# Kernel optimization log

Hardware: AMD Instinct MI355X
Metric: run time of the kernel (lower is better)

The kernel has to match this reference:

```python
import jax, jax.numpy as jnp
import numpy as np

N, F_IN, UNITS, HEADS = 4096, 128, 64, 4
EDGE_P = 0.01  # adjacency density


def setup_inputs() -> dict:
    key = jax.random.key(0)
    k1, k2, k3, k4, k5 = jax.random.split(key, 5)
    inputs = jax.random.normal(k1, (N, F_IN), dtype=jnp.float32)
    adj = jax.random.bernoulli(k2, EDGE_P, (N, N)).astype(jnp.float32)
    # glorot-normal-ish parameter scales
    w = jax.random.normal(k3, (F_IN, UNITS), dtype=jnp.float32) * np.float32(np.sqrt(2.0 / (F_IN + UNITS)))
    attn_w1 = jax.random.normal(k4, (UNITS, HEADS), dtype=jnp.float32) * np.float32(np.sqrt(2.0 / (UNITS + HEADS)))
    attn_w2 = jax.random.normal(k5, (UNITS, HEADS), dtype=jnp.float32) * np.float32(np.sqrt(2.0 / (UNITS + HEADS)))
    return {"inputs": inputs, "adj": adj, "w": w, "attn_w1": attn_w1, "attn_w2": attn_w2}


def reference(inputs, adj, w, attn_w1, attn_w2):
    # dropout=0, bias=0, final_layer=False, activation=relu
    x = inputs @ w                                  # [N, U]
    e1 = x @ attn_w1                                # [N, H]
    e2 = x @ attn_w2                                # [N, H]
    # coeffs[i, j, h] = relu(e1[i, h] + e2[j, h])
    coeffs = jax.nn.relu(e1[:, None, :] + e2[None, :, :])   # [N, N, H]
    # NOTE: original multiplies by adj (zeros -> logit 0, not -inf) then softmax over j
    scores = adj[:, :, None] * coeffs               # [N, N, H]
    attn = jax.nn.softmax(scores, axis=1)           # normalize over neighbors j
    # per-head aggregation, concat heads -> [N, H*U] (head-major blocks)
    out = jnp.einsum("ijh,ju->ihu", attn, x).reshape(N, HEADS * UNITS)
    return jax.nn.relu(out)
```

## Files before the change

kernel.cpp:

```cpp
#include <hip/hip_runtime.h>

#define N_NODES 4096
#define F_IN    128
#define UNITS   64
#define HEADS   4
#define ROWS_PB 4
#define GRID1   (N_NODES / ROWS_PB)
#define NBR_CAP 128

__global__ __launch_bounds__(256, 4) void k1(
        const float* __restrict__ inputs, const float* __restrict__ adj,
        const float* __restrict__ w, const float* __restrict__ aw1,
        const float* __restrict__ aw2, float* __restrict__ x,
        float* __restrict__ e1g, float* __restrict__ e2g,
        float* __restrict__ S, int* __restrict__ cnt_g,
        unsigned short* __restrict__ nbr_g)
{
    __shared__ float w_lds[F_IN * UNITS];
    __shared__ float in_lds[ROWS_PB * F_IN];
    __shared__ float x_lds[ROWS_PB * 65];
    __shared__ unsigned short nbr_lds[ROWS_PB * NBR_CAP];

    const int t    = threadIdx.x;
    const int lane = t & 63;
    const int wid  = t >> 6;
    const int row0 = blockIdx.x * ROWS_PB;
    const int r    = row0 + wid;

    {
        const float4* src = (const float4*)w;
        float4* dst = (float4*)w_lds;
        for (int idx = t; idx < F_IN * UNITS / 4; idx += 256) dst[idx] = src[idx];
    }
    if (t < ROWS_PB * F_IN / 4)
        ((float4*)in_lds)[t] = ((const float4*)(inputs + (size_t)row0 * F_IN))[t];
    __syncthreads();

    const float4* arow = (const float4*)(adj + (size_t)r * N_NODES);
    float4 av[16];
#pragma unroll
    for (int j = 0; j < 16; j++) av[j] = arow[lane + 64 * j];

    float acc = 0.f;
    const float4* ir = (const float4*)(in_lds + wid * F_IN);
#pragma unroll 8
    for (int c = 0; c < F_IN / 4; c++) {
        const float4 a = ir[c];
        const int k4 = c * 4;
        acc = fmaf(a.x, w_lds[(k4 + 0) * UNITS + lane],
              fmaf(a.y, w_lds[(k4 + 1) * UNITS + lane],
              fmaf(a.z, w_lds[(k4 + 2) * UNITS + lane],
              fmaf(a.w, w_lds[(k4 + 3) * UNITS + lane], acc))));
    }
    x_lds[wid * 65 + lane] = acc;
    x[(size_t)r * UNITS + lane] = acc;

    int off = 0;
    const unsigned long long lt = (1ull << lane) - 1ull;
#pragma unroll
    for (int j = 0; j < 16; j++) {
        const int gbase = 4 * (lane + 64 * j);
        unsigned long long bm;
        bm = __ballot(av[j].x != 0.f);
        if (av[j].x != 0.f) { const int p = off + __popcll(bm & lt);
            if (p < NBR_CAP) nbr_lds[wid * NBR_CAP + p] = (unsigned short)(gbase + 0); }
        off += __popcll(bm);
        bm = __ballot(av[j].y != 0.f);
        if (av[j].y != 0.f) { const int p = off + __popcll(bm & lt);
            if (p < NBR_CAP) nbr_lds[wid * NBR_CAP + p] = (unsigned short)(gbase + 1); }
        off += __popcll(bm);
        bm = __ballot(av[j].z != 0.f);
        if (av[j].z != 0.f) { const int p = off + __popcll(bm & lt);
            if (p < NBR_CAP) nbr_lds[wid * NBR_CAP + p] = (unsigned short)(gbase + 2); }
        off += __popcll(bm);
        bm = __ballot(av[j].w != 0.f);
        if (av[j].w != 0.f) { const int p = off + __popcll(bm & lt);
            if (p < NBR_CAP) nbr_lds[wid * NBR_CAP + p] = (unsigned short)(gbase + 3); }
        off += __popcll(bm);
    }
    const int cntc = min(off, NBR_CAP);
    if (lane == 0) cnt_g[r] = cntc;
    for (int idx = lane; idx < cntc; idx += 64)
        nbr_g[(size_t)r * NBR_CAP + idx] = nbr_lds[wid * NBR_CAP + idx];

    __syncthreads();

    if (t < 32) {
        const int rr = t >> 3;
        const int rem = t & 7;
        const int h = rem & 3;
        const bool first = rem < 4;
        const float* aw = first ? aw1 : aw2;
        float s = 0.f;
#pragma unroll 8
        for (int uu = 0; uu < UNITS; uu++)
            s += x_lds[rr * 65 + uu] * aw[uu * HEADS + h];
        (first ? e1g : e2g)[(size_t)(row0 + rr) * HEADS + h] = s;
    }
    if (t < 64) {
        const float s = x_lds[0 * 65 + t] + x_lds[1 * 65 + t]
                      + x_lds[2 * 65 + t] + x_lds[3 * 65 + t];
        atomicAdd(&S[t], s);
    }
}

__global__ __launch_bounds__(256) void k2(
        const float* __restrict__ x, const float* __restrict__ e1g,
        const float* __restrict__ e2g, const float* __restrict__ S,
        const int* __restrict__ cnt_g, const unsigned short* __restrict__ nbr_g,
        float* __restrict__ out)
{
    __shared__ unsigned short nb[NBR_CAP];
    __shared__ float4 wgt[NBR_CAP];
    __shared__ float red[4][HEADS * UNITS];
    __shared__ float4 denred[4];

    const int i = blockIdx.x;
    const int t = threadIdx.x;
    const int lane = t & 63;
    const int wid = t >> 6;

    const int n = min(cnt_g[i], NBR_CAP);
    const float4 e1v = *(const float4*)(e1g + (size_t)i * HEADS);

    if (t < n) {
        const int j = nbr_g[(size_t)i * NBR_CAP + t];
        nb[t] = (unsigned short)j;
        const float4 e2v = *(const float4*)(e2g + (size_t)j * HEADS);
        float4 wv;
        wv.x = __expf(fmaxf(e1v.x + e2v.x, 0.f)) - 1.f;
        wv.y = __expf(fmaxf(e1v.y + e2v.y, 0.f)) - 1.f;
        wv.z = __expf(fmaxf(e1v.z + e2v.z, 0.f)) - 1.f;
        wv.w = __expf(fmaxf(e1v.w + e2v.w, 0.f)) - 1.f;
        wgt[t] = wv;
    }
    __syncthreads();

    float a0 = 0.f, a1 = 0.f, a2 = 0.f, a3 = 0.f;
    float dx = 0.f, dy = 0.f, dz = 0.f, dw = 0.f;
    for (int k = wid; k < n; k += 4) {
        const float4 p = wgt[k];
        const int j = nb[k];
        const float xv = x[(j << 6) + lane];
        a0 = fmaf(p.x, xv, a0);
        a1 = fmaf(p.y, xv, a1);
        a2 = fmaf(p.z, xv, a2);
        a3 = fmaf(p.w, xv, a3);
        dx += p.x; dy += p.y; dz += p.z; dw += p.w;
    }
    red[wid][0 * 64 + lane] = a0;
    red[wid][1 * 64 + lane] = a1;
    red[wid][2 * 64 + lane] = a2;
    red[wid][3 * 64 + lane] = a3;
    if (lane == 0) denred[wid] = make_float4(dx, dy, dz, dw);
    __syncthreads();

    const float accsum = red[0][t] + red[1][t] + red[2][t] + red[3][t];
    const float den = ((const float*)&denred[0])[wid]
                    + ((const float*)&denred[1])[wid]
                    + ((const float*)&denred[2])[wid]
                    + ((const float*)&denred[3])[wid];
    out[(size_t)i * (HEADS * UNITS) + t] =
        fmaxf((S[lane] + accsum) / ((float)N_NODES + den), 0.f);
}

extern "C" void kernel_launch(void* const* d_in, const int* in_sizes, int n_in,
                              void* d_out, int out_size, void* d_ws, size_t ws_size,
                              hipStream_t stream) {
    const float* inputs = (const float*)d_in[0];
    const float* adj    = (const float*)d_in[1];
    const float* w      = (const float*)d_in[2];
    const float* aw1    = (const float*)d_in[3];
    const float* aw2    = (const float*)d_in[4];
    float* out = (float*)d_out;

    float* ws = (float*)d_ws;
    float* x   = ws;
    float* e1  = ws + 262144;
    float* e2  = ws + 262144 + 16384;
    float* S   = ws + 262144 + 2 * 16384;
    int*   cnt = (int*)(ws + 262144 + 2 * 16384 + 64);
    unsigned short* nbr = (unsigned short*)(ws + 262144 + 2 * 16384 + 64 + 4096);

    hipMemsetAsync(S, 0, UNITS * sizeof(float), stream);
    k1<<<GRID1, 256, 0, stream>>>(inputs, adj, w, aw1, aw2, x, e1, e2, S, cnt, nbr);
    k2<<<N_NODES, 256, 0, stream>>>(x, e1, e2, S, cnt, nbr, out);
}
```

Baseline: 137.5 us.

## Split projection and adjacency scan into interleaved heterogeneous blocks

The first kernel now runs two kinds of blocks in one grid. One in five blocks does the 4-row feature projection plus the attention-logit and column-sum work. The other blocks each compact the neighbour list of a single adjacency row using all 256 threads, with a shared atomic counter assigning offsets per wave. The aim is to spread the large adjacency read over more, shorter blocks and decouple it from the GEMM work. The cost is that each block still reserves the shared-memory union sized for the GEMM path, so fewer adjacency rows may be in flight per CU. Neighbour order inside a row also becomes nondeterministic across waves.

```diff
diff --git a/kernel.cpp b/kernel.cpp
--- a/kernel.cpp
+++ b/kernel.cpp
@@ -5,10 +5,14 @@
 #define UNITS   64
 #define HEADS   4
 #define ROWS_PB 4
-#define GRID1   (N_NODES / ROWS_PB)
+#define GRID_GEMM (N_NODES / ROWS_PB)
+#define GRID_A  (GRID_GEMM + N_NODES)
 #define NBR_CAP 128
 
-__global__ __launch_bounds__(256, 4) void k1(
+struct GemmS { float w[F_IN * UNITS]; float in[ROWS_PB * F_IN]; float xl[ROWS_PB * 65]; };
+struct ScanS { unsigned short nbr[NBR_CAP]; };
+
+__global__ __launch_bounds__(256) void kA(
         const float* __restrict__ inputs, const float* __restrict__ adj,
         const float* __restrict__ w, const float* __restrict__ aw1,
         const float* __restrict__ aw2, float* __restrict__ x,
@@ -16,95 +20,121 @@
         float* __restrict__ S, int* __restrict__ cnt_g,
         unsigned short* __restrict__ nbr_g)
 {
-    __shared__ float w_lds[F_IN * UNITS];
-    __shared__ float in_lds[ROWS_PB * F_IN];
-    __shared__ float x_lds[ROWS_PB * 65];
-    __shared__ unsigned short nbr_lds[ROWS_PB * NBR_CAP];
-
+    __shared__ union { GemmS g; ScanS s; } u;
+    __shared__ int cnt;
+
+    const int bid  = blockIdx.x;
     const int t    = threadIdx.x;
     const int lane = t & 63;
     const int wid  = t >> 6;
-    const int row0 = blockIdx.x * ROWS_PB;
-    const int r    = row0 + wid;
-
-    {
-        const float4* src = (const float4*)w;
-        float4* dst = (float4*)w_lds;
-        for (int idx = t; idx < F_IN * UNITS / 4; idx += 256) dst[idx] = src[idx];
-    }
-    if (t < ROWS_PB * F_IN / 4)
-        ((float4*)in_lds)[t] = ((const float4*)(inputs + (size_t)row0 * F_IN))[t];
-    __syncthreads();
-
-    const float4* arow = (const float4*)(adj + (size_t)r * N_NODES);
-    float4 av[16];
-#pragma unroll
-    for (int j = 0; j < 16; j++) av[j] = arow[lane + 64 * j];
-
-    float acc = 0.f;
-    const float4* ir = (const float4*)(in_lds + wid * F_IN);
+
+    if (bid % 5 == 0) {
+        const int row0 = (bid / 5) * ROWS_PB;
+
+        {
+            const float4* src = (const float4*)w;
+            float4* dst = (float4*)u.g.w;
+            for (int idx = t; idx < F_IN * UNITS / 4; idx += 256) dst[idx] = src[idx];
+        }
+        if (t < ROWS_PB * F_IN / 4)
+            ((float4*)u.g.in)[t] = ((const float4*)(inputs + (size_t)row0 * F_IN))[t];
+        __syncthreads();
+
+        float acc = 0.f;
+        const float4* ir = (const float4*)(u.g.in + wid * F_IN);
 #pragma unroll 8
-    for (int c = 0; c < F_IN / 4; c++) {
-        const float4 a = ir[c];
-        const int k4 = c * 4;
-        acc = fmaf(a.x, w_lds[(k4 + 0) * UNITS + lane],
-              fmaf(a.y, w_lds[(k4 + 1) * UNITS + lane],
-              fmaf(a.z, w_lds[(k4 + 2) * UNITS + lane],
-              fmaf(a.w, w_lds[(k4 + 3) * UNITS + lane], acc))));
-    }
-    x_lds[wid * 65 + lane] = acc;
-    x[(size_t)r * UNITS + lane] = acc;
-
-    int off = 0;
-    const unsigned long long lt = (1ull << lane) - 1ull;
-#pragma unroll
-    for (int j = 0; j < 16; j++) {
-        const int gbase = 4 * (lane + 64 * j);
-        unsigned long long bm;
-        bm = __ballot(av[j].x != 0.f);
-        if (av[j].x != 0.f) { const int p = off + __popcll(bm & lt);
-            if (p < NBR_CAP) nbr_lds[wid * NBR_CAP + p] = (unsigned short)(gbase + 0); }
-        off += __popcll(bm);
-        bm = __ballot(av[j].y != 0.f);
-        if (av[j].y != 0.f) { const int p = off + __popcll(bm & lt);
-            if (p < NBR_CAP) nbr_lds[wid * NBR_CAP + p] = (unsigned short)(gbase + 1); }
-        off += __popcll(bm);
-        bm = __ballot(av[j].z != 0.f);
-        if (av[j].z != 0.f) { const int p = off + __popcll(bm & lt);
-            if (p < NBR_CAP) nbr_lds[wid * NBR_CAP + p] = (unsigned short)(gbase + 2); }
-        off += __popcll(bm);
-        bm = __ballot(av[j].w != 0.f);
-        if (av[j].w != 0.f) { const int p = off + __popcll(bm & lt);
-            if (p < NBR_CAP) nbr_lds[wid * NBR_CAP + p] = (unsigned short)(gbase + 3); }
-        off += __popcll(bm);
-    }
-    const int cntc = min(off, NBR_CAP);
-    if (lane == 0) cnt_g[r] = cntc;
-    for (int idx = lane; idx < cntc; idx += 64)
-        nbr_g[(size_t)r * NBR_CAP + idx] = nbr_lds[wid * NBR_CAP + idx];
-
-    __syncthreads();
-
-    if (t < 32) {
-        const int rr = t >> 3;
-        const int rem = t & 7;
-        const int h = rem & 3;
-        const bool first = rem < 4;
-        const float* aw = first ? aw1 : aw2;
-        float s = 0.f;
+        for (int c = 0; c < F_IN / 4; c++) {
+            const float4 a = ir[c];
+            const int k4 = c * 4;
+            acc = fmaf(a.x, u.g.w[(k4 + 0) * UNITS + lane],
+                  fmaf(a.y, u.g.w[(k4 + 1) * UNITS + lane],
+                  fmaf(a.z, u.g.w[(k4 + 2) * UNITS + lane],
+                  fmaf(a.w, u.g.w[(k4 + 3) * UNITS + lane], acc))));
+        }
+        u.g.xl[wid * 65 + lane] = acc;
+        x[(size_t)(row0 + wid) * UNITS + lane] = acc;
+        __syncthreads();
+
+        if (t < 32) {
+            const int rr = t >> 3;
+            const int rem = t & 7;
+            const int h = rem & 3;
+            const bool first = rem < 4;
+            const float* aw = first ? aw1 : aw2;
+            float s = 0.f;
 #pragma unroll 8
-        for (int uu = 0; uu < UNITS; uu++)
-            s += x_lds[rr * 65 + uu] * aw[uu * HEADS + h];
-        (first ? e1g : e2g)[(size_t)(row0 + rr) * HEADS + h] = s;
-    }
-    if (t < 64) {
-        const float s = x_lds[0 * 65 + t] + x_lds[1 * 65 + t]
-                      + x_lds[2 * 65 + t] + x_lds[3 * 65 + t];
-        atomicAdd(&S[t], s);
+            for (int uu = 0; uu < UNITS; uu++)
+                s += u.g.xl[rr * 65 + uu] * aw[uu * HEADS + h];
+            (first ? e1g : e2g)[(size_t)(row0 + rr) * HEADS + h] = s;
+        }
+        if (t < 64) {
+            const float s = u.g.xl[0 * 65 + t] + u.g.xl[1 * 65 + t]
+                          + u.g.xl[2 * 65 + t] + u.g.xl[3 * 65 + t];
+            atomicAdd(&S[t], s);
+        }
+    } else {
+        const int i = bid - bid / 5 - 1;
+
+        if (t == 0) cnt = 0;
+        __syncthreads();
+
+        const float4* arow = (const float4*)(adj + (size_t)i * N_NODES);
+        const float4 v0 = arow[t];
+        const float4 v1 = arow[t + 256];
+        const float4 v2 = arow[t + 512];
+        const float4 v3 = arow[t + 768];
+
+        const unsigned long long b0  = __ballot(v0.x != 0.f);
+        const unsigned long long b1  = __ballot(v0.y != 0.f);
+        const unsigned long long b2  = __ballot(v0.z != 0.f);
+        const unsigned long long b3  = __ballot(v0.w != 0.f);
+        const unsigned long long b4  = __ballot(v1.x != 0.f);
+        const unsigned long long b5  = __ballot(v1.y != 0.f);
+        const unsigned long long b6  = __ballot(v1.z != 0.f);
+        const unsigned long long b7  = __ballot(v1.w != 0.f);
+        const unsigned long long b8  = __ballot(v2.x != 0.f);
+        const unsigned long long b9  = __ballot(v2.y != 0.f);
+        const unsigned long long b10 = __ballot(v2.z != 0.f);
+        const unsigned long long b11 = __ballot(v2.w != 0.f);
+        const unsigned long long b12 = __ballot(v3.x != 0.f);
+        const unsigned long long b13 = __ballot(v3.y != 0.f);
+        const unsigned long long b14 = __ballot(v3.z != 0.f);
+        const unsigned long long b15 = __ballot(v3.w != 0.f);
+
+        const int tot = __popcll(b0) + __popcll(b1) + __popcll(b2) + __popcll(b3)
+                      + __popcll(b4) + __popcll(b5) + __popcll(b6) + __popcll(b7)
+                      + __popcll(b8) + __popcll(b9) + __popcll(b10) + __popcll(b11)
+                      + __popcll(b12) + __popcll(b13) + __popcll(b14) + __popcll(b15);
+
+        int wbase = 0;
+        if (lane == 0) wbase = atomicAdd(&cnt, tot);
+        wbase = __shfl(wbase, 0);
+
+        const unsigned long long lt = (1ull << lane) - 1ull;
+        int off = wbase;
+        const int g0 = t * 4, g1 = (t + 256) * 4, g2 = (t + 512) * 4, g3 = (t + 768) * 4;
+#define EMIT(val, bm, gidx) \
+        do { if ((val) != 0.f) { const int p_ = off + __popcll((bm) & lt); \
+             if (p_ < NBR_CAP) u.s.nbr[p_] = (unsigned short)(gidx); } \
+             off += __popcll(bm); } while (0)
+        EMIT(v0.x, b0,  g0 + 0); EMIT(v0.y, b1,  g0 + 1);
+        EMIT(v0.z, b2,  g0 + 2); EMIT(v0.w, b3,  g0 + 3);
+        EMIT(v1.x, b4,  g1 + 0); EMIT(v1.y, b5,  g1 + 1);
+        EMIT(v1.z, b6,  g1 + 2); EMIT(v1.w, b7,  g1 + 3);
+        EMIT(v2.x, b8,  g2 + 0); EMIT(v2.y, b9,  g2 + 1);
+        EMIT(v2.z, b10, g2 + 2); EMIT(v2.w, b11, g2 + 3);
+        EMIT(v3.x, b12, g3 + 0); EMIT(v3.y, b13, g3 + 1);
+        EMIT(v3.z, b14, g3 + 2); EMIT(v3.w, b15, g3 + 3);
+#undef EMIT
+        __syncthreads();
+
+        const int n = min(cnt, NBR_CAP);
+        if (t < n) nbr_g[(size_t)i * NBR_CAP + t] = u.s.nbr[t];
+        if (t == 0) cnt_g[i] = n;
     }
 }
 
-__global__ __launch_bounds__(256) void k2(
+__global__ __launch_bounds__(256) void kB(
         const float* __restrict__ x, const float* __restrict__ e1g,
         const float* __restrict__ e2g, const float* __restrict__ S,
         const int* __restrict__ cnt_g, const unsigned short* __restrict__ nbr_g,
@@ -183,6 +213,6 @@
     unsigned short* nbr = (unsigned short*)(ws + 262144 + 2 * 16384 + 64 + 4096);
 
     hipMemsetAsync(S, 0, UNITS * sizeof(float), stream);
-    k1<<<GRID1, 256, 0, stream>>>(inputs, adj, w, aw1, aw2, x, e1, e2, S, cnt, nbr);
-    k2<<<N_NODES, 256, 0, stream>>>(x, e1, e2, S, cnt, nbr, out);
+    kA<<<GRID_A, 256, 0, stream>>>(inputs, adj, w, aw1, aw2, x, e1, e2, S, cnt, nbr);
+    kB<<<N_NODES, 256, 0, stream>>>(x, e1, e2, S, cnt, nbr, out);
 }
```

After: 134.5 us. 2.1% less time.
